# Kernel tuning notes

Measured on AMD Instinct MI355X. Metric: run time of the kernel, lower is better.

The kernel has to match this reference:

```python
import jax, jax.numpy as jnp
import numpy as np

N_NODES = 20000
N_EDGES = 320000
IN_DIM = 128
HID = 64
HEADS = 4
NEG_SLOPE = 0.2  # PyG GATConv default


def _glorot(key, shape):
    fan_in, fan_out = shape[0], shape[-1]
    lim = jnp.sqrt(6.0 / (fan_in + fan_out))
    return jax.random.uniform(key, shape, jnp.float32, -lim, lim)


def setup_inputs() -> dict:
    key = jax.random.key(0)
    ks = jax.random.split(key, 16)
    x = jax.random.normal(ks[0], (N_NODES, IN_DIM), jnp.float32)
    edge_index = jax.random.randint(ks[1], (2, N_EDGES), 0, N_NODES, dtype=jnp.int64)
    # layer 1: in=128 -> heads=4, out=64, concat
    W1 = _glorot(ks[2], (IN_DIM, HEADS * HID))
    a_src1 = _glorot(ks[3], (HEADS, HID))
    a_dst1 = _glorot(ks[4], (HEADS, HID))
    b1 = jnp.zeros((HEADS * HID,), jnp.float32)
    # layer 2: in=256 -> heads=4, out=64, concat
    W2 = _glorot(ks[5], (HEADS * HID, HEADS * HID))
    a_src2 = _glorot(ks[6], (HEADS, HID))
    a_dst2 = _glorot(ks[7], (HEADS, HID))
    b2 = jnp.zeros((HEADS * HID,), jnp.float32)
    # layer 3: in=256 -> heads=1, out=1, mean (concat=False)
    W3 = _glorot(ks[8], (HEADS * HID, 1))
    a_src3 = _glorot(ks[9], (1, 1))
    a_dst3 = _glorot(ks[10], (1, 1))
    b3 = jnp.zeros((1,), jnp.float32)
    return {
        "x": x, "edge_index": edge_index,
        "W1": W1, "a_src1": a_src1, "a_dst1": a_dst1, "b1": b1,
        "W2": W2, "a_src2": a_src2, "a_dst2": a_dst2, "b2": b2,
        "W3": W3, "a_src3": a_src3, "a_dst3": a_dst3, "b3": b3,
    }


def gat_conv(x, src, dst, W, a_src, a_dst, b, heads, out_c, concat):
    """PyG GATConv (add_self_loops already applied to src/dst)."""
    n = x.shape[0]
    h = (x @ W).reshape(n, heads, out_c)            # [N,H,C]
    alpha_s = jnp.sum(h * a_src, axis=-1)           # [N,H]
    alpha_d = jnp.sum(h * a_dst, axis=-1)           # [N,H]
    e = jax.nn.leaky_relu(alpha_s[src] + alpha_d[dst], NEG_SLOPE)  # [E,H]
    # segment softmax over incoming edges of each destination node
    e_max = jax.ops.segment_max(e, dst, num_segments=n)            # [N,H]
    ex = jnp.exp(e - e_max[dst])                                   # [E,H]
    denom = jax.ops.segment_sum(ex, dst, num_segments=n)           # [N,H]
    alpha = ex / denom[dst]                                        # [E,H]
    msg = h[src] * alpha[:, :, None]                               # [E,H,C]
    out = jax.ops.segment_sum(msg, dst, num_segments=n)            # [N,H,C]
    if concat:
        out = out.reshape(n, heads * out_c)
    else:
        out = out.mean(axis=1)
    return out + b


def reference(x, edge_index, W1, a_src1, a_dst1, b1, W2, a_src2, a_dst2, b2,
              W3, a_src3, a_dst3, b3):
    n = x.shape[0]
    loops = jnp.arange(n, dtype=edge_index.dtype)
    src = jnp.concatenate([edge_index[0], loops])
    dst = jnp.concatenate([edge_index[1], loops])
    h = jax.nn.elu(gat_conv(x, src, dst, W1, a_src1, a_dst1, b1, HEADS, HID, True))
    # dropout is identity in eval mode
    h = jax.nn.elu(gat_conv(h, src, dst, W2, a_src2, a_dst2, b2, HEADS, HID, True))
    h = gat_conv(h, src, dst, W3, a_src3, a_dst3, b3, 1, 1, False)
    return h.reshape(-1)
```

## Files before the change

### kernel.cpp

```cpp
#include <hip/hip_runtime.h>
#include <hip/hip_bf16.h>
#include <cmath>

#define N_NODESC 20000
#define E_RAW    320000
#define E_TOTC   340000
#define HEADSC   4
#define FC       256
#define NEG_SLOPE 0.2f

typedef __attribute__((ext_vector_type(8))) short short8v;
typedef __attribute__((ext_vector_type(4))) float f32x4;

__device__ __forceinline__ int dstOf(const int* ei, int e) {
  return (e < E_RAW) ? ei[E_RAW + e] : (e - E_RAW);
}
__device__ __forceinline__ int srcOf(const int* ei, int e) {
  return (e < E_RAW) ? ei[e] : (e - E_RAW);
}
__device__ __forceinline__ float lrelu(float v) { return v > 0.f ? v : NEG_SLOPE * v; }

__device__ __forceinline__ unsigned short f2bf(float f) {
  __hip_bfloat16 h = __float2bfloat16(f);
  return reinterpret_cast<unsigned short&>(h);
}
__device__ __forceinline__ float bf2f(unsigned short u) {
  return __uint_as_float(((unsigned int)u) << 16);
}

__device__ __forceinline__ void atomicMaxF(float* addr, float val) {
  if (val >= 0.f) atomicMax((int*)addr, __float_as_int(val));
  else            atomicMin((unsigned int*)addr, (unsigned int)__float_as_int(val));
}

__global__ void mega_prep(const float* __restrict__ x,
                          unsigned short* __restrict__ xhi, unsigned short* __restrict__ xlo,
                          const float* __restrict__ W1,
                          unsigned short* __restrict__ w1hi, unsigned short* __restrict__ w1lo,
                          const float* __restrict__ W2,
                          unsigned short* __restrict__ w2hi, unsigned short* __restrict__ w2lo,
                          int* __restrict__ deg, float* __restrict__ amax) {
  const int bid = blockIdx.x, t = threadIdx.x;
  if (bid < 10000) {
    int i = bid * 256 + t;
    float v = x[i];
    unsigned short hh = f2bf(v);
    xhi[i] = hh; xlo[i] = f2bf(v - bf2f(hh));
  } else if (bid < 10128) {
    int idx = (bid - 10000) * 256 + t;
    int c = idx >> 7, k = idx & 127;
    float v = W1[k * FC + c];
    unsigned short hh = f2bf(v);
    w1hi[c * 128 + k] = hh; w1lo[c * 128 + k] = f2bf(v - bf2f(hh));
  } else if (bid < 10384) {
    int idx = (bid - 10128) * 256 + t;
    int c = idx >> 8, k = idx & 255;
    float v = W2[k * FC + c];
    unsigned short hh = f2bf(v);
    w2hi[c * 256 + k] = hh; w2lo[c * 256 + k] = f2bf(v - bf2f(hh));
  } else {
    int i = (bid - 10384) * 256 + t;
    if (i < N_NODESC) deg[i] = 0;
    else if (i < N_NODESC + 8) amax[i - N_NODESC] = -INFINITY;
  }
}

template<int K>
__global__ void __launch_bounds__(256) mfma_gemm(
    const unsigned short* __restrict__ Ahi, const unsigned short* __restrict__ Alo,
    const unsigned short* __restrict__ WhiT, const unsigned short* __restrict__ WloT,
    const float* __restrict__ a_src, const float* __restrict__ a_dst,
    unsigned short* __restrict__ hb, float* __restrict__ as, float* __restrict__ ad,
    float* __restrict__ asmax) {
  __shared__ unsigned short xsh[32 * K];
  __shared__ unsigned short xsl[32 * K];
  __shared__ float asred[32][4];
  __shared__ float adred[32][4];
  __shared__ float wmax[2][4];
  const int t = threadIdx.x;
  const int w = t >> 6, l = t & 63;
  const int n0 = blockIdx.x * 32;
  const int r16 = l & 15;
  const int kq = l >> 4;
  const int col0 = w * 64;

  const int KC = K / 8;
  for (int c = t; c < 32 * KC; c += 256) {
    int row = c / KC, k16 = c - row * KC;
    int bo = (row * K + k16 * 8) * 2;
    int swz = bo ^ ((row & 7) << 4);
    *(short8v*)((char*)xsh + swz) = *(const short8v*)(Ahi + (long)(n0 + row) * K + k16 * 8);
    *(short8v*)((char*)xsl + swz) = *(const short8v*)(Alo + (long)(n0 + row) * K + k16 * 8);
  }
  __syncthreads();

  f32x4 acc[2][4];
#pragma unroll
  for (int rt = 0; rt < 2; ++rt)
#pragma unroll
    for (int ct = 0; ct < 4; ++ct) acc[rt][ct] = f32x4{0.f, 0.f, 0.f, 0.f};

  for (int ks = 0; ks < K; ks += 32) {
    const int kb = ks + kq * 8;
    short8v aHi[2], aLo[2];
#pragma unroll
    for (int rt = 0; rt < 2; ++rt) {
      int bo = ((rt * 16 + r16) * K + kb) * 2;
      int swz = bo ^ ((r16 & 7) << 4);
      aHi[rt] = *(const short8v*)((const char*)xsh + swz);
      aLo[rt] = *(const short8v*)((const char*)xsl + swz);
    }
#pragma unroll
    for (int ct = 0; ct < 4; ++ct) {
      const long wrow = (long)(col0 + ct * 16 + r16) * K + kb;
      short8v wHi = *(const short8v*)(WhiT + wrow);
      short8v wLo = *(const short8v*)(WloT + wrow);
#pragma unroll
      for (int rt = 0; rt < 2; ++rt) {
        acc[rt][ct] = __builtin_amdgcn_mfma_f32_16x16x32_bf16(aHi[rt], wHi, acc[rt][ct], 0, 0, 0);
        acc[rt][ct] = __builtin_amdgcn_mfma_f32_16x16x32_bf16(aHi[rt], wLo, acc[rt][ct], 0, 0, 0);
        acc[rt][ct] = __builtin_amdgcn_mfma_f32_16x16x32_bf16(aLo[rt], wHi, acc[rt][ct], 0, 0, 0);
      }
    }
  }

  float asv[4], adv[4];
#pragma unroll
  for (int ct = 0; ct < 4; ++ct) {
    int c = col0 + ct * 16 + r16;
    asv[ct] = a_src[c];
    adv[ct] = a_dst[c];
  }
#pragma unroll
  for (int rt = 0; rt < 2; ++rt) {
#pragma unroll
    for (int j = 0; j < 4; ++j) {
      const int r = rt * 16 + kq * 4 + j;
      const int g = n0 + r;
#pragma unroll
      for (int ct = 0; ct < 4; ++ct)
        hb[(long)g * FC + col0 + ct * 16 + r16] = f2bf(acc[rt][ct][j]);
      float ps = acc[rt][0][j] * asv[0] + acc[rt][1][j] * asv[1]
               + acc[rt][2][j] * asv[2] + acc[rt][3][j] * asv[3];
      float pd = acc[rt][0][j] * adv[0] + acc[rt][1][j] * adv[1]
               + acc[rt][2][j] * adv[2] + acc[rt][3][j] * adv[3];
      for (int off = 8; off; off >>= 1) {
        ps += __shfl_down(ps, off, 16);
        pd += __shfl_down(pd, off, 16);
      }
      if (r16 == 0) {
        asred[r][w] = ps;
        adred[r][w] = pd;
      }
    }
  }
  __syncthreads();
  if (t < 128) {
    const int rr = t >> 2, hh = t & 3;
    const int g = n0 + rr;
    float va = asred[rr][hh];
    as[(long)g * HEADSC + hh] = va;
    ad[(long)g * HEADSC + hh] = adred[rr][hh];
    float mv = va;
    for (int off = 32; off >= 4; off >>= 1) mv = fmaxf(mv, __shfl_down(mv, off, 64));
    if (l < 4) wmax[t >> 6][l] = mv;
  }
  __syncthreads();
  if (t < 4) atomicMaxF(&asmax[t], fmaxf(wmax[0][t], wmax[1][t]));
}

__global__ void deg_count(const int* __restrict__ ei, int* __restrict__ deg) {
  int e = blockIdx.x * 256 + threadIdx.x;
  if (e >= E_TOTC) return;
  atomicAdd(&deg[dstOf(ei, e)], 1);
}

__global__ void scan_kernel(const int* __restrict__ deg, int* __restrict__ row_ptr,
                            int* __restrict__ cursor) {
  const int t = threadIdx.x;
  const int lane = t & 63, wid = t >> 6;
  const int PER = (N_NODESC + 1023) / 1024;
  const int base = t * PER;
  int own = 0;
  for (int i = 0; i < PER; ++i) {
    int idx = base + i;
    if (idx < N_NODESC) own += deg[idx];
  }
  int inc = own;
  for (int off = 1; off < 64; off <<= 1) {
    int v = __shfl_up(inc, off, 64);
    if (lane >= off) inc += v;
  }
  __shared__ int wtot[16], woff[16];
  if (lane == 63) wtot[wid] = inc;
  __syncthreads();
  if (t == 0) {
    int r = 0;
    for (int i = 0; i < 16; ++i) { woff[i] = r; r += wtot[i]; }
  }
  __syncthreads();
  int run = woff[wid] + inc - own;
  for (int i = 0; i < PER; ++i) {
    int idx = base + i;
    if (idx < N_NODESC) {
      row_ptr[idx] = run;
      cursor[idx]  = run;
      run += deg[idx];
    }
  }
  if (t == 1023) row_ptr[N_NODESC] = run;
}

__global__ void fill_kernel(const int* __restrict__ ei, int* __restrict__ cursor,
                            int* __restrict__ col_src) {
  int e = blockIdx.x * 256 + threadIdx.x;
  if (e >= E_TOTC) return;
  int d = dstOf(ei, e);
  int pos = atomicAdd(&cursor[d], 1);
  col_src[pos] = srcOf(ei, e);
}

template<int MODE>
__global__ void __launch_bounds__(256) fused_sa(
    const int* __restrict__ row_ptr, const int* __restrict__ col_src,
    const float* __restrict__ asf, const float4* __restrict__ ad4,
    const float* __restrict__ asmax,
    const unsigned short* __restrict__ hb, const float* __restrict__ b,
    unsigned short* __restrict__ out_hi, unsigned short* __restrict__ out_lo,
    const float* __restrict__ W3, const float* __restrict__ asc3,
    const float* __restrict__ adc3, float* __restrict__ h3,
    float* __restrict__ a3s, float* __restrict__ a3d) {
  const int l = threadIdx.x & 63, wv = threadIdx.x >> 6;
  const int d = blockIdx.x * 4 + wv;
  const int h = l >> 4;
  const int j0 = row_ptr[d], j1 = row_ptr[d + 1];
  const float4 adv = ad4[d];
  const float advh = (h == 0) ? adv.x : (h == 1) ? adv.y : (h == 2) ? adv.z : adv.w;
  const float mh = lrelu(asmax[h] + advh);

  const ushort4* hb4 = (const ushort4*)hb;
  float a0 = 0.f, a1 = 0.f, a2 = 0.f, a3 = 0.f, sm = 0.f;
  int j = j0;
  for (; j + 8 <= j1; j += 8) {
    int     s[8];
    float   av[8];
    ushort4 v[8];
#pragma unroll
    for (int u = 0; u < 8; ++u) s[u] = col_src[j + u];
#pragma unroll
    for (int u = 0; u < 8; ++u) av[u] = asf[s[u] * 4 + h];
#pragma unroll
    for (int u = 0; u < 8; ++u) v[u] = hb4[(long)s[u] * 64 + l];
#pragma unroll
    for (int u = 0; u < 8; ++u) {
      float e = expf(lrelu(av[u] + advh) - mh);
      sm += e;
      a0 = fmaf(e, bf2f(v[u].x), a0);
      a1 = fmaf(e, bf2f(v[u].y), a1);
      a2 = fmaf(e, bf2f(v[u].z), a2);
      a3 = fmaf(e, bf2f(v[u].w), a3);
    }
  }
  for (; j < j1; ++j) {
    int s = col_src[j];
    float e = expf(lrelu(asf[s * 4 + h] + advh) - mh);
    ushort4 v = hb4[(long)s * 64 + l];
    sm += e;
    a0 = fmaf(e, bf2f(v.x), a0);
    a1 = fmaf(e, bf2f(v.y), a1);
    a2 = fmaf(e, bf2f(v.z), a2);
    a3 = fmaf(e, bf2f(v.w), a3);
  }
  const float dn = 1.f / sm;
  float4 bb = *(const float4*)(b + 4 * l);
  float o0 = a0 * dn + bb.x;
  float o1 = a1 * dn + bb.y;
  float o2 = a2 * dn + bb.z;
  float o3 = a3 * dn + bb.w;
  o0 = o0 > 0.f ? o0 : expm1f(o0);
  o1 = o1 > 0.f ? o1 : expm1f(o1);
  o2 = o2 > 0.f ? o2 : expm1f(o2);
  o3 = o3 > 0.f ? o3 : expm1f(o3);

  if (MODE == 0) {
    ushort4 hi, lo;
    hi.x = f2bf(o0); lo.x = f2bf(o0 - bf2f(hi.x));
    hi.y = f2bf(o1); lo.y = f2bf(o1 - bf2f(hi.y));
    hi.z = f2bf(o2); lo.z = f2bf(o2 - bf2f(hi.z));
    hi.w = f2bf(o3); lo.w = f2bf(o3 - bf2f(hi.w));
    ((ushort4*)out_hi)[(long)d * 64 + l] = hi;
    ((ushort4*)out_lo)[(long)d * 64 + l] = lo;
  } else {
    float4 w3 = *(const float4*)(W3 + 4 * l);
    float p = o0 * w3.x + o1 * w3.y + o2 * w3.z + o3 * w3.w;
    for (int off = 32; off; off >>= 1) p += __shfl_down(p, off, 64);
    if (l == 0) {
      h3[d]  = p;
      a3s[d] = p * asc3[0];
      a3d[d] = p * adc3[0];
    }
  }
}

__global__ void __launch_bounds__(256) fused_sa3(
    const int* __restrict__ row_ptr, const int* __restrict__ col_src,
    const float* __restrict__ as, const float* __restrict__ ad,
    const float* __restrict__ h3, const float* __restrict__ b3,
    float* __restrict__ out) {
  const int wv = threadIdx.x >> 6, l = threadIdx.x & 63;
  const int d = blockIdx.x * 4 + wv;
  if (d >= N_NODESC) return;
  const int j0 = row_ptr[d], j1 = row_ptr[d + 1];
  const float adv = ad[d];
  float mx = -INFINITY;
  for (int j = j0 + l; j < j1; j += 64)
    mx = fmaxf(mx, lrelu(as[col_src[j]] + adv));
  for (int off = 32; off; off >>= 1) mx = fmaxf(mx, __shfl_xor(mx, off, 64));
  float sm = 0.f, acc = 0.f;
  for (int j = j0 + l; j < j1; j += 64) {
    int s = col_src[j];
    float e = expf(lrelu(as[s] + adv) - mx);
    sm += e;
    acc = fmaf(e, h3[s], acc);
  }
  for (int off = 32; off; off >>= 1) {
    sm  += __shfl_xor(sm, off, 64);
    acc += __shfl_xor(acc, off, 64);
  }
  if (l == 0) out[d] = acc / sm + b3[0];
}

extern "C" void kernel_launch(void* const* d_in, const int* in_sizes, int n_in,
                              void* d_out, int out_size, void* d_ws, size_t ws_size,
                              hipStream_t stream) {
  const float* x    = (const float*)d_in[0];
  const int*   ei   = (const int*)d_in[1];
  const float* W1   = (const float*)d_in[2];
  const float* as1  = (const float*)d_in[3];
  const float* ad1  = (const float*)d_in[4];
  const float* b1   = (const float*)d_in[5];
  const float* W2   = (const float*)d_in[6];
  const float* as2  = (const float*)d_in[7];
  const float* ad2  = (const float*)d_in[8];
  const float* b2   = (const float*)d_in[9];
  const float* W3   = (const float*)d_in[10];
  const float* as3  = (const float*)d_in[11];
  const float* ad3  = (const float*)d_in[12];
  const float* b3   = (const float*)d_in[13];
  float* out = (float*)d_out;

  float* ws = (float*)d_ws;
  size_t off = 0;
  float* wAs   = ws + off; off += (size_t)N_NODESC * HEADSC;
  float* wAd   = ws + off; off += (size_t)N_NODESC * HEADSC;
  float* h3    = ws + off; off += N_NODESC;
  float* a3s   = ws + off; off += N_NODESC;
  float* a3d   = ws + off; off += N_NODESC;
  float* amax  = ws + off; off += 8;
  int* deg     = (int*)(ws + off); off += N_NODESC;
  int* row_ptr = (int*)(ws + off); off += N_NODESC + 1;
  int* cursor  = (int*)(ws + off); off += N_NODESC;
  int* col_src = (int*)(ws + off); off += E_TOTC;
  off = (off + 3) & ~(size_t)3;
  unsigned short* hb     = (unsigned short*)(ws + off); off += (size_t)N_NODESC * 128;
  unsigned short* act_hi = (unsigned short*)(ws + off); off += (size_t)N_NODESC * 128;
  unsigned short* act_lo = (unsigned short*)(ws + off); off += (size_t)N_NODESC * 128;
  unsigned short* xhi    = (unsigned short*)(ws + off); off += (size_t)N_NODESC * 64;
  unsigned short* xlo    = (unsigned short*)(ws + off); off += (size_t)N_NODESC * 64;
  unsigned short* W1hiT  = (unsigned short*)(ws + off); off += 16384;
  unsigned short* W1loT  = (unsigned short*)(ws + off); off += 16384;
  unsigned short* W2hiT  = (unsigned short*)(ws + off); off += 32768;
  unsigned short* W2loT  = (unsigned short*)(ws + off); off += 32768;

  const int gridE  = (E_TOTC + 255) / 256;
  const int gridN4 = (N_NODESC + 3) / 4;
  const int gemmG  = N_NODESC / 32;

  mega_prep<<<10463, 256, 0, stream>>>(x, xhi, xlo, W1, W1hiT, W1loT,
                                       W2, W2hiT, W2loT, deg, amax);
  deg_count<<<gridE, 256, 0, stream>>>(ei, deg);
  scan_kernel<<<1, 1024, 0, stream>>>(deg, row_ptr, cursor);
  fill_kernel<<<gridE, 256, 0, stream>>>(ei, cursor, col_src);

  mfma_gemm<128><<<gemmG, 256, 0, stream>>>(xhi, xlo, W1hiT, W1loT, as1, ad1,
                                            hb, wAs, wAd, amax);
  fused_sa<0><<<N_NODESC / 4, 256, 0, stream>>>(row_ptr, col_src, wAs, (const float4*)wAd,
                                                amax, hb, b1, act_hi, act_lo,
                                                nullptr, nullptr, nullptr, nullptr, nullptr, nullptr);

  mfma_gemm<256><<<gemmG, 256, 0, stream>>>(act_hi, act_lo, W2hiT, W2loT, as2, ad2,
                                            hb, wAs, wAd, amax + 4);
  fused_sa<1><<<N_NODESC / 4, 256, 0, stream>>>(row_ptr, col_src, wAs, (const float4*)wAd,
                                                amax + 4, hb, b2, nullptr, nullptr,
                                                W3, as3, ad3, h3, a3s, a3d);

  fused_sa3<<<gridN4, 256, 0, stream>>>(row_ptr, col_src, a3s, a3d, h3, b3, out);
}
```

Before: 222.2 us.

## Split hidden features into per-head planes and aggregate one head per block

The GEMM epilogue now writes its bf16 output in a head-major layout, one [N,64] plane per head. The aggregation kernel gives each block a single head, so each gather reads a 128-byte contiguous row slice from a 2.5MB plane instead of 512-byte rows from a 10MB array. The aim is better cache locality for the random source gathers. In exchange, every edge's col_src and attention-score reads are repeated four times, the grid is four times larger, and a small extra kernel is needed to sum the per-head partial layer-3 projections.

Measured after the change: 281.7 us. +26.8%, slower.

```diff
diff --git a/kernel.cpp b/kernel.cpp
--- a/kernel.cpp
+++ b/kernel.cpp
@@ -139,7 +139,7 @@
       const int g = n0 + r;
 #pragma unroll
       for (int ct = 0; ct < 4; ++ct)
-        hb[(long)g * FC + col0 + ct * 16 + r16] = f2bf(acc[rt][ct][j]);
+        hb[((long)w * N_NODESC + g) * 64 + ct * 16 + r16] = f2bf(acc[rt][ct][j]);
       float ps = acc[rt][0][j] * asv[0] + acc[rt][1][j] * asv[1]
                + acc[rt][2][j] * asv[2] + acc[rt][3][j] * asv[3];
       float pd = acc[rt][0][j] * adv[0] + acc[rt][1][j] * adv[1]
@@ -223,83 +223,69 @@
 template<int MODE>
 __global__ void __launch_bounds__(256) fused_sa(
     const int* __restrict__ row_ptr, const int* __restrict__ col_src,
-    const float* __restrict__ asf, const float4* __restrict__ ad4,
+    const float* __restrict__ asf, const float* __restrict__ adf,
     const float* __restrict__ asmax,
     const unsigned short* __restrict__ hb, const float* __restrict__ b,
     unsigned short* __restrict__ out_hi, unsigned short* __restrict__ out_lo,
-    const float* __restrict__ W3, const float* __restrict__ asc3,
-    const float* __restrict__ adc3, float* __restrict__ h3,
-    float* __restrict__ a3s, float* __restrict__ a3d) {
+    const float* __restrict__ W3, float* __restrict__ h3p) {
   const int l = threadIdx.x & 63, wv = threadIdx.x >> 6;
-  const int d = blockIdx.x * 4 + wv;
-  const int h = l >> 4;
+  const int h = blockIdx.x & 3;
+  const int d = (blockIdx.x >> 2) * 4 + wv;
   const int j0 = row_ptr[d], j1 = row_ptr[d + 1];
-  const float4 adv = ad4[d];
-  const float advh = (h == 0) ? adv.x : (h == 1) ? adv.y : (h == 2) ? adv.z : adv.w;
+  const float advh = adf[d * 4 + h];
   const float mh = lrelu(asmax[h] + advh);
 
-  const ushort4* hb4 = (const ushort4*)hb;
-  float a0 = 0.f, a1 = 0.f, a2 = 0.f, a3 = 0.f, sm = 0.f;
+  const unsigned short* hbh = hb + (long)h * N_NODESC * 64;
+  float acc = 0.f, sm = 0.f;
   int j = j0;
   for (; j + 8 <= j1; j += 8) {
-    int     s[8];
-    float   av[8];
-    ushort4 v[8];
+    int            s[8];
+    float          av[8];
+    unsigned short v[8];
 #pragma unroll
     for (int u = 0; u < 8; ++u) s[u] = col_src[j + u];
 #pragma unroll
     for (int u = 0; u < 8; ++u) av[u] = asf[s[u] * 4 + h];
 #pragma unroll
-    for (int u = 0; u < 8; ++u) v[u] = hb4[(long)s[u] * 64 + l];
+    for (int u = 0; u < 8; ++u) v[u] = hbh[(long)s[u] * 64 + l];
 #pragma unroll
     for (int u = 0; u < 8; ++u) {
       float e = expf(lrelu(av[u] + advh) - mh);
       sm += e;
-      a0 = fmaf(e, bf2f(v[u].x), a0);
-      a1 = fmaf(e, bf2f(v[u].y), a1);
-      a2 = fmaf(e, bf2f(v[u].z), a2);
-      a3 = fmaf(e, bf2f(v[u].w), a3);
+      acc = fmaf(e, bf2f(v[u]), acc);
     }
   }
   for (; j < j1; ++j) {
     int s = col_src[j];
     float e = expf(lrelu(asf[s * 4 + h] + advh) - mh);
-    ushort4 v = hb4[(long)s * 64 + l];
+    unsigned short v = hbh[(long)s * 64 + l];
     sm += e;
-    a0 = fmaf(e, bf2f(v.x), a0);
-    a1 = fmaf(e, bf2f(v.y), a1);
-    a2 = fmaf(e, bf2f(v.z), a2);
-    a3 = fmaf(e, bf2f(v.w), a3);
-  }
-  const float dn = 1.f / sm;
-  float4 bb = *(const float4*)(b + 4 * l);
-  float o0 = a0 * dn + bb.x;
-  float o1 = a1 * dn + bb.y;
-  float o2 = a2 * dn + bb.z;
-  float o3 = a3 * dn + bb.w;
-  o0 = o0 > 0.f ? o0 : expm1f(o0);
-  o1 = o1 > 0.f ? o1 : expm1f(o1);
-  o2 = o2 > 0.f ? o2 : expm1f(o2);
-  o3 = o3 > 0.f ? o3 : expm1f(o3);
+    acc = fmaf(e, bf2f(v), acc);
+  }
+  float o = acc / sm + b[h * 64 + l];
+  o = o > 0.f ? o : expm1f(o);
 
   if (MODE == 0) {
-    ushort4 hi, lo;
-    hi.x = f2bf(o0); lo.x = f2bf(o0 - bf2f(hi.x));
-    hi.y = f2bf(o1); lo.y = f2bf(o1 - bf2f(hi.y));
-    hi.z = f2bf(o2); lo.z = f2bf(o2 - bf2f(hi.z));
-    hi.w = f2bf(o3); lo.w = f2bf(o3 - bf2f(hi.w));
-    ((ushort4*)out_hi)[(long)d * 64 + l] = hi;
-    ((ushort4*)out_lo)[(long)d * 64 + l] = lo;
+    unsigned short hi = f2bf(o);
+    unsigned short lo = f2bf(o - bf2f(hi));
+    out_hi[(long)d * FC + h * 64 + l] = hi;
+    out_lo[(long)d * FC + h * 64 + l] = lo;
   } else {
-    float4 w3 = *(const float4*)(W3 + 4 * l);
-    float p = o0 * w3.x + o1 * w3.y + o2 * w3.z + o3 * w3.w;
+    float p = o * W3[h * 64 + l];
     for (int off = 32; off; off >>= 1) p += __shfl_down(p, off, 64);
-    if (l == 0) {
-      h3[d]  = p;
-      a3s[d] = p * asc3[0];
-      a3d[d] = p * adc3[0];
-    }
-  }
+    if (l == 0) h3p[(long)h * N_NODESC + d] = p;
+  }
+}
+
+__global__ void h3_combine(const float* __restrict__ h3p, const float* __restrict__ asc3,
+                           const float* __restrict__ adc3, float* __restrict__ h3,
+                           float* __restrict__ a3s, float* __restrict__ a3d) {
+  int i = blockIdx.x * 256 + threadIdx.x;
+  if (i >= N_NODESC) return;
+  float s = h3p[i] + h3p[N_NODESC + i] + h3p[2 * N_NODESC + i] + h3p[3 * N_NODESC + i];
+  h3[i]  = s;
+  a3s[i] = s * asc3[0];
+  a3d[i] = s * adc3[0];
 }
 
 __global__ void __launch_bounds__(256) fused_sa3(
@@ -356,6 +342,7 @@
   float* h3    = ws + off; off += N_NODESC;
   float* a3s   = ws + off; off += N_NODESC;
   float* a3d   = ws + off; off += N_NODESC;
+  float* h3p   = ws + off; off += (size_t)N_NODESC * HEADSC;
   float* amax  = ws + off; off += 8;
   int* deg     = (int*)(ws + off); off += N_NODESC;
   int* row_ptr = (int*)(ws + off); off += N_NODESC + 1;
@@ -373,6 +360,7 @@
   unsigned short* W2loT  = (unsigned short*)(ws + off); off += 32768;
 
   const int gridE  = (E_TOTC + 255) / 256;
+  const int gridN  = (N_NODESC + 255) / 256;
   const int gridN4 = (N_NODESC + 3) / 4;
   const int gemmG  = N_NODESC / 32;
 
@@ -384,15 +372,14 @@
 
   mfma_gemm<128><<<gemmG, 256, 0, stream>>>(xhi, xlo, W1hiT, W1loT, as1, ad1,
                                             hb, wAs, wAd, amax);
-  fused_sa<0><<<N_NODESC / 4, 256, 0, stream>>>(row_ptr, col_src, wAs, (const float4*)wAd,
-                                                amax, hb, b1, act_hi, act_lo,
-                                                nullptr, nullptr, nullptr, nullptr, nullptr, nullptr);
+  fused_sa<0><<<N_NODESC, 256, 0, stream>>>(row_ptr, col_src, wAs, wAd, amax,
+                                            hb, b1, act_hi, act_lo, nullptr, nullptr);
 
   mfma_gemm<256><<<gemmG, 256, 0, stream>>>(act_hi, act_lo, W2hiT, W2loT, as2, ad2,
                                             hb, wAs, wAd, amax + 4);
-  fused_sa<1><<<N_NODESC / 4, 256, 0, stream>>>(row_ptr, col_src, wAs, (const float4*)wAd,
-                                                amax + 4, hb, b2, nullptr, nullptr,
-                                                W3, as3, ad3, h3, a3s, a3d);
+  fused_sa<1><<<N_NODESC, 256, 0, stream>>>(row_ptr, col_src, wAs, wAd, amax + 4,
+                                            hb, b2, nullptr, nullptr, W3, h3p);
+  h3_combine<<<gridN, 256, 0, stream>>>(h3p, as3, ad3, h3, a3s, a3d);
 
   fused_sa3<<<gridN4, 256, 0, stream>>>(row_ptr, col_src, a3s, a3d, h3, b3, out);
 }
```
